# Kernel optimization log

Measured on AMD Instinct MI355X. Metric: run time of the kernel, lower is better.

The kernel has to match this reference:

```python
import jax, jax.numpy as jnp
import numpy as np


def _conv1d(x, kernel, bias):
    # Keras Conv1D, padding='valid', stride 1. x: (b, ts, c); kernel: (K, c, f)
    y = jax.lax.conv_general_dilated(x, kernel, (1,), 'VALID',
                                     dimension_numbers=('NWC', 'WIO', 'NWC'))
    return y + bias


def setup_inputs() -> dict:
    key = jax.random.key(0)
    k1, k2, k3 = jax.random.split(key, 3)
    KSIZE, C, F = 5, 32, 32
    x = jax.random.normal(k1, (16, 65536, C), jnp.float32)
    Wconv = jax.random.normal(k2, (KSIZE, C, F), jnp.float32) * 0.05
    bconv = jnp.zeros((F,), jnp.float32)
    Wdef = jax.random.normal(k3, (KSIZE, 1), jnp.float32) * 0.1
    return {"x": x, "Wconv": Wconv, "bconv": bconv, "Wdef": Wdef}


def reference(x, Wconv, bconv, Wdef):
    K = Wconv.shape[0]
    # regularGrid: R = [-floor(K/2), ..., K-1-floor(K/2)]
    R = jnp.arange(K, dtype=jnp.float32) - (K // 2)
    offset = _conv1d(x, Wconv, bconv)                 # (b, ts-K+1, f)
    # dpn = mean over all positions of (offset + R) -> mean(offset) + R, shape (K,)
    pn = jnp.mean(offset) + R
    # g(Q, Q+pn) = max(0, 1 - |Q - (Q+pn)|) = max(0, 1 - |pn|): constant per tap
    scale = jnp.maximum(0.0, 1.0 - jnp.abs(pn))       # (K,)
    # y_k = scale_k * flatten(x); sum_k W_k * y_k == x * sum_k(W_k * scale_k)
    s = jnp.sum(Wdef[:, 0] * scale)                   # scalar
    y = x * s                                         # (b, ts, c)
    return _conv1d(y, Wconv, bconv)                   # (b, ts-K+1, f)
```

## Files before the change

kernel.cpp:

```cpp
#include <hip/hip_runtime.h>
#include <hip/hip_fp16.h>

#define T    65536
#define TOUT 65532
#define NB   16
#define CH   32
#define NF   32
#define KS   5
#define BM   128
#define NCHB 1024

typedef _Float16 f16x8 __attribute__((ext_vector_type(8)));
typedef _Float16 f16x4 __attribute__((ext_vector_type(4)));
typedef float    f32x4 __attribute__((ext_vector_type(4)));
typedef float    f32x4v __attribute__((ext_vector_type(4)));


__device__ __forceinline__ f16x4 cvt4(float4 v) {
    f16x4 h;
    h[0] = (_Float16)v.x; h[1] = (_Float16)v.y;
    h[2] = (_Float16)v.z; h[3] = (_Float16)v.w;
    return h;
}
__device__ __forceinline__ f16x4 cvt4v(f32x4v v) {
    f16x4 h;
    h[0] = (_Float16)v[0]; h[1] = (_Float16)v[1];
    h[2] = (_Float16)v[2]; h[3] = (_Float16)v[3];
    return h;
}

template <bool WRITE_XH>
__global__ __launch_bounds__(256) void chsum6_kernel(const float* __restrict__ x,
                                                     _Float16* __restrict__ xh,
                                                     float* __restrict__ partials) {
    __shared__ float tot[CH];
    const int tid  = threadIdx.x;
    const int lane = tid & 63;
    if (tid < CH) tot[tid] = 0.f;
    __syncthreads();

    const f32x4v* x4  = (const f32x4v*)x;
    f16x4*        xh4 = (f16x4*)xh;
    const size_t base = (size_t)blockIdx.x * 8192;
    float s0 = 0.f, s1 = 0.f, s2 = 0.f, s3 = 0.f;
#pragma unroll 8
    for (int q = 0; q < 32; ++q) {
        size_t i = base + (size_t)q * 256 + tid;
        f32x4v v = __builtin_nontemporal_load(&x4[i]);
        s0 += v[0]; s1 += v[1]; s2 += v[2]; s3 += v[3];
        if (WRITE_XH) xh4[i] = cvt4v(v);
    }
#pragma unroll
    for (int m = 8; m <= 32; m <<= 1) {
        s0 += __shfl_xor(s0, m, 64);
        s1 += __shfl_xor(s1, m, 64);
        s2 += __shfl_xor(s2, m, 64);
        s3 += __shfl_xor(s3, m, 64);
    }
    if (lane < 8) {
        const int cc = lane * 4;
        atomicAdd(&tot[cc + 0], s0);
        atomicAdd(&tot[cc + 1], s1);
        atomicAdd(&tot[cc + 2], s2);
        atomicAdd(&tot[cc + 3], s3);
    }
    __syncthreads();
    if (tid < CH) partials[(size_t)blockIdx.x * CH + tid] = tot[tid];
}

__global__ __launch_bounds__(256) void scalar2_kernel(const float* __restrict__ x,
                                                      const float* __restrict__ Wconv,
                                                      const float* __restrict__ bconv,
                                                      const float* __restrict__ Wdef,
                                                      const float* __restrict__ partials,
                                                      float* __restrict__ ws) {
    __shared__ float ltot[CH];
    __shared__ float hb[4][CH], tb[4][CH];
    __shared__ float partial[256];
    const int tid = threadIdx.x;
    if (tid < CH) ltot[tid] = 0.f;
    __syncthreads();
    {
        const float4* p4 = (const float4*)partials;
        float s0 = 0.f, s1 = 0.f, s2 = 0.f, s3 = 0.f;
#pragma unroll 8
        for (int i = 0; i < 32; ++i) {
            float4 v = p4[i * 256 + tid];
            s0 += v.x; s1 += v.y; s2 += v.z; s3 += v.w;
        }
        int cc = (tid & 7) * 4;
        atomicAdd(&ltot[cc + 0], s0);
        atomicAdd(&ltot[cc + 1], s1);
        atomicAdd(&ltot[cc + 2], s2);
        atomicAdd(&ltot[cc + 3], s3);
    }
    {
        int j = tid >> 5, c = tid & 31;
        int row = (j < 4) ? j : (T - 8 + j);
        float e = 0.f;
        for (int bb = 0; bb < NB; ++bb)
            e += x[((size_t)bb * T + row) * CH + c];
        if (j < 4) hb[j][c] = e; else tb[j - 4][c] = e;
    }
    __syncthreads();

    float term = 0.f;
    if (tid < KS * CH) {
        int k = tid >> 5, c = tid & 31;
        float wf = 0.f;
        const float* wp = &Wconv[(size_t)tid * NF];
        for (int f = 0; f < NF; ++f) wf += wp[f];
        float S = ltot[c];
        for (int jj = 0; jj < k; ++jj) S -= hb[jj][c];
        for (int jj = k; jj < 4; ++jj) S -= tb[jj][c];
        term = wf * S;
    }
    partial[tid] = term;
    __syncthreads();
    for (int off = 128; off > 0; off >>= 1) {
        if (tid < off) partial[tid] += partial[tid + off];
        __syncthreads();
    }
    if (tid == 0) {
        float sum_b = 0.f;
        for (int f = 0; f < NF; ++f) sum_b += bconv[f];
        float mean_off = partial[0] / (float)((size_t)NB * TOUT * NF) + sum_b / (float)NF;
        float s = 0.f;
        for (int k = 0; k < KS; ++k) {
            float pn = mean_off + (float)(k - 2);
            s += Wdef[k] * fmaxf(0.f, 1.f - fabsf(pn));
        }
        ws[CH] = s;
    }
}

__global__ __launch_bounds__(256) void conv2_kernel(const _Float16* __restrict__ xh,
                                                    const float* __restrict__ Wconv,
                                                    const float* __restrict__ bconv,
                                                    const float* __restrict__ ws,
                                                    float* __restrict__ out) {
    __shared__ _Float16 A[(BM + 4) * 40];
    __shared__ _Float16 Wt[KS * CH * 40];

    const int tid = threadIdx.x;
    const int b   = blockIdx.y;
    const int t0  = blockIdx.x * BM;
    const int c0  = (tid & 7) * 4;

    {
        const f16x4* xh4 = (const f16x4*)xh;
        for (int r = (tid >> 3); r < BM + 4; r += 32) {
            int t = t0 + r;
            f16x4 h = {};
            if (t < T) h = xh4[((size_t)b * T + t) * 8 + (tid & 7)];
            *(f16x4*)&A[r * 40 + c0] = h;
        }
    }
    {
        const float4* w4 = (const float4*)Wconv;
#pragma unroll
        for (int j = 0; j < 5; ++j) {
            int i4 = tid + j * 256;
            float4 v = w4[i4];
            int fi = i4 * 4;
            int k = fi >> 10, c = (fi >> 5) & 31, f = fi & 31;
            _Float16* wrow = &Wt[(k * CH + f) * 40 + c];
            wrow[0 * 40] = (_Float16)v.x;
            wrow[1 * 40] = (_Float16)v.y;
            wrow[2 * 40] = (_Float16)v.z;
            wrow[3 * 40] = (_Float16)v.w;
        }
    }
    __syncthreads();

    const int lane = tid & 63;
    const int wave = tid >> 6;
    const int rowbase = wave * 32;
    const int lrow = lane & 15;
    const int kgrp = lane >> 4;

    f32x4 acc00 = {}, acc01 = {}, acc10 = {}, acc11 = {};
#pragma unroll
    for (int kk = 0; kk < KS; ++kk) {
        f16x8 a0 = *(const f16x8*)&A[(rowbase + lrow + kk) * 40 + kgrp * 8];
        f16x8 a1 = *(const f16x8*)&A[(rowbase + 16 + lrow + kk) * 40 + kgrp * 8];
        f16x8 b0 = *(const f16x8*)&Wt[(kk * CH + lrow) * 40 + kgrp * 8];
        f16x8 b1 = *(const f16x8*)&Wt[(kk * CH + 16 + lrow) * 40 + kgrp * 8];
        acc00 = __builtin_amdgcn_mfma_f32_16x16x32_f16(a0, b0, acc00, 0, 0, 0);
        acc01 = __builtin_amdgcn_mfma_f32_16x16x32_f16(a0, b1, acc01, 0, 0, 0);
        acc10 = __builtin_amdgcn_mfma_f32_16x16x32_f16(a1, b0, acc10, 0, 0, 0);
        acc11 = __builtin_amdgcn_mfma_f32_16x16x32_f16(a1, b1, acc11, 0, 0, 0);
    }

    float sv  = ws[CH];
    int col0  = lane & 15;
    float bc0 = bconv[col0], bc1 = bconv[col0 + 16];
    int rbase = rowbase + ((lane >> 4) << 2);
#pragma unroll
    for (int reg = 0; reg < 4; ++reg) {
        int t = t0 + rbase + reg;
        if (t < TOUT) {
            float* o = &out[((size_t)b * TOUT + t) * NF];
            o[col0]      = sv * acc00[reg] + bc0;
            o[col0 + 16] = sv * acc01[reg] + bc1;
        }
        int t1 = t + 16;
        if (t1 < TOUT) {
            float* o = &out[((size_t)b * TOUT + t1) * NF];
            o[col0]      = sv * acc10[reg] + bc0;
            o[col0 + 16] = sv * acc11[reg] + bc1;
        }
    }
}

__global__ __launch_bounds__(256) void conv_kernel(const float* __restrict__ x,
                                                   const float* __restrict__ Wconv,
                                                   const float* __restrict__ bconv,
                                                   const float* __restrict__ ws,
                                                   float* __restrict__ out) {
    __shared__ _Float16 A[(BM + 4) * 40];
    __shared__ _Float16 Wt[KS * CH * 40];
    int tid = threadIdx.x;
    int b   = blockIdx.y;
    int t0  = blockIdx.x * BM;
    {
        int c0 = (tid & 7) * 4;
        for (int r = (tid >> 3); r < BM + 4; r += 32) {
            int t = t0 + r;
            float4 v = make_float4(0.f, 0.f, 0.f, 0.f);
            if (t < T) v = *(const float4*)&x[((size_t)b * T + t) * CH + c0];
            *(f16x4*)&A[r * 40 + c0] = cvt4(v);
        }
    }
    if (tid < KS * CH) {
        int k = tid >> 5, c = tid & 31;
        const float* wp = &Wconv[(size_t)tid * NF];
        for (int f = 0; f < NF; ++f)
            Wt[(k * CH + f) * 40 + c] = (_Float16)wp[f];
    }
    __syncthreads();
    int lane = tid & 63;
    int wave = tid >> 6;
    int rowbase = wave * 32;
    int lrow = lane & 15;
    int kgrp = lane >> 4;
    f32x4 acc00 = {}, acc01 = {}, acc10 = {}, acc11 = {};
#pragma unroll
    for (int kk = 0; kk < KS; ++kk) {
        f16x8 a0 = *(const f16x8*)&A[(rowbase + lrow + kk) * 40 + kgrp * 8];
        f16x8 a1 = *(const f16x8*)&A[(rowbase + 16 + lrow + kk) * 40 + kgrp * 8];
        f16x8 b0 = *(const f16x8*)&Wt[(kk * CH + lrow) * 40 + kgrp * 8];
        f16x8 b1 = *(const f16x8*)&Wt[(kk * CH + 16 + lrow) * 40 + kgrp * 8];
        acc00 = __builtin_amdgcn_mfma_f32_16x16x32_f16(a0, b0, acc00, 0, 0, 0);
        acc01 = __builtin_amdgcn_mfma_f32_16x16x32_f16(a0, b1, acc01, 0, 0, 0);
        acc10 = __builtin_amdgcn_mfma_f32_16x16x32_f16(a1, b0, acc10, 0, 0, 0);
        acc11 = __builtin_amdgcn_mfma_f32_16x16x32_f16(a1, b1, acc11, 0, 0, 0);
    }
    float sv  = ws[CH];
    int col0  = lane & 15;
    float bc0 = bconv[col0], bc1 = bconv[col0 + 16];
    int rbase = rowbase + ((lane >> 4) << 2);
#pragma unroll
    for (int reg = 0; reg < 4; ++reg) {
        int t = t0 + rbase + reg;
        if (t < TOUT) {
            float* o = &out[((size_t)b * TOUT + t) * NF];
            o[col0]      = sv * acc00[reg] + bc0;
            o[col0 + 16] = sv * acc01[reg] + bc1;
        }
        int t1 = t + 16;
        if (t1 < TOUT) {
            float* o = &out[((size_t)b * TOUT + t1) * NF];
            o[col0]      = sv * acc10[reg] + bc0;
            o[col0 + 16] = sv * acc11[reg] + bc1;
        }
    }
}

extern "C" void kernel_launch(void* const* d_in, const int* in_sizes, int n_in,
                              void* d_out, int out_size, void* d_ws, size_t ws_size,
                              hipStream_t stream) {
    const float* x     = (const float*)d_in[0];
    const float* Wconv = (const float*)d_in[1];
    const float* bconv = (const float*)d_in[2];
    const float* Wdef  = (const float*)d_in[3];
    float* out      = (float*)d_out;
    float* ws       = (float*)d_ws;
    float* partials = ws + 64;
    _Float16* xh    = (_Float16*)((char*)d_ws + 524288);

    const size_t need = 524288 + (size_t)NB * T * CH * sizeof(_Float16);
    dim3 grid((TOUT + BM - 1) / BM, NB);

    if (ws_size >= need) {
        chsum6_kernel<true><<<dim3(NCHB), dim3(256), 0, stream>>>(x, xh, partials);
        scalar2_kernel<<<dim3(1), dim3(256), 0, stream>>>(x, Wconv, bconv, Wdef, partials, ws);
        conv2_kernel<<<grid, dim3(256), 0, stream>>>(xh, Wconv, bconv, ws, out);
    } else {
        chsum6_kernel<false><<<dim3(NCHB), dim3(256), 0, stream>>>(x, xh, partials);
        scalar2_kernel<<<dim3(1), dim3(256), 0, stream>>>(x, Wconv, bconv, Wdef, partials, ws);
        conv_kernel<<<grid, dim3(256), 0, stream>>>(x, Wconv, bconv, ws, out);
    }
}
```

Measured before the change: 80.62 us.

## Process two row tiles per conv block with register prefetch; double channel-sum blocks

Measured after the change: 78.53 us. -2.6%, faster.

```diff
diff --git a/kernel.cpp b/kernel.cpp
--- a/kernel.cpp
+++ b/kernel.cpp
@@ -8,7 +8,7 @@
 #define NF   32
 #define KS   5
 #define BM   128
-#define NCHB 1024
+#define NCHB 2048
 
 typedef _Float16 f16x8 __attribute__((ext_vector_type(8)));
 typedef _Float16 f16x4 __attribute__((ext_vector_type(4)));
@@ -41,10 +41,10 @@
 
     const f32x4v* x4  = (const f32x4v*)x;
     f16x4*        xh4 = (f16x4*)xh;
-    const size_t base = (size_t)blockIdx.x * 8192;
+    const size_t base = (size_t)blockIdx.x * 4096;
     float s0 = 0.f, s1 = 0.f, s2 = 0.f, s3 = 0.f;
 #pragma unroll 8
-    for (int q = 0; q < 32; ++q) {
+    for (int q = 0; q < 16; ++q) {
         size_t i = base + (size_t)q * 256 + tid;
         f32x4v v = __builtin_nontemporal_load(&x4[i]);
         s0 += v[0]; s1 += v[1]; s2 += v[2]; s3 += v[3];
@@ -84,7 +84,7 @@
         const float4* p4 = (const float4*)partials;
         float s0 = 0.f, s1 = 0.f, s2 = 0.f, s3 = 0.f;
 #pragma unroll 8
-        for (int i = 0; i < 32; ++i) {
+        for (int i = 0; i < 64; ++i) {
             float4 v = p4[i * 256 + tid];
             s0 += v.x; s1 += v.y; s2 += v.z; s3 += v.w;
         }
@@ -134,7 +134,7 @@
     }
 }
 
-__global__ __launch_bounds__(256) void conv2_kernel(const _Float16* __restrict__ xh,
+__global__ __launch_bounds__(256) void conv3_kernel(const _Float16* __restrict__ xh,
                                                     const float* __restrict__ Wconv,
                                                     const float* __restrict__ bconv,
                                                     const float* __restrict__ ws,
@@ -144,18 +144,36 @@
 
     const int tid = threadIdx.x;
     const int b   = blockIdx.y;
-    const int t0  = blockIdx.x * BM;
+    const int t0  = blockIdx.x * (2 * BM);
     const int c0  = (tid & 7) * 4;
-
-    {
-        const f16x4* xh4 = (const f16x4*)xh;
-        for (int r = (tid >> 3); r < BM + 4; r += 32) {
-            int t = t0 + r;
-            f16x4 h = {};
-            if (t < T) h = xh4[((size_t)b * T + t) * 8 + (tid & 7)];
-            *(f16x4*)&A[r * 40 + c0] = h;
-        }
-    }
+    const int g8  = tid & 7;
+    const int srow = tid >> 3;
+
+    const f16x4* xh4 = (const f16x4*)xh;
+    const size_t rowb = (size_t)b * T * 8;
+
+    f16x4 ra0, ra1, ra2, ra3, ra4;
+    auto LOADA = [&](int sub) {
+        int tbase = t0 + sub * BM + srow;
+        ra0 = xh4[rowb + (size_t)(tbase      ) * 8 + g8];
+        ra1 = xh4[rowb + (size_t)(tbase + 32 ) * 8 + g8];
+        ra2 = xh4[rowb + (size_t)(tbase + 64 ) * 8 + g8];
+        ra3 = xh4[rowb + (size_t)(tbase + 96 ) * 8 + g8];
+        if (tid < 32) {
+            int t = t0 + sub * BM + 128 + srow;
+            ra4 = (t < T) ? xh4[rowb + (size_t)t * 8 + g8] : (f16x4){};
+        }
+    };
+    auto WRITEA = [&]() {
+        *(f16x4*)&A[(srow      ) * 40 + c0] = ra0;
+        *(f16x4*)&A[(srow + 32 ) * 40 + c0] = ra1;
+        *(f16x4*)&A[(srow + 64 ) * 40 + c0] = ra2;
+        *(f16x4*)&A[(srow + 96 ) * 40 + c0] = ra3;
+        if (tid < 32)
+            *(f16x4*)&A[(128 + srow) * 40 + c0] = ra4;
+    };
+
+    LOADA(0);
     {
         const float4* w4 = (const float4*)Wconv;
 #pragma unroll
@@ -171,6 +189,7 @@
             wrow[3 * 40] = (_Float16)v.w;
         }
     }
+    WRITEA();
     __syncthreads();
 
     const int lane = tid & 63;
@@ -178,37 +197,48 @@
     const int rowbase = wave * 32;
     const int lrow = lane & 15;
     const int kgrp = lane >> 4;
-
-    f32x4 acc00 = {}, acc01 = {}, acc10 = {}, acc11 = {};
-#pragma unroll
-    for (int kk = 0; kk < KS; ++kk) {
-        f16x8 a0 = *(const f16x8*)&A[(rowbase + lrow + kk) * 40 + kgrp * 8];
-        f16x8 a1 = *(const f16x8*)&A[(rowbase + 16 + lrow + kk) * 40 + kgrp * 8];
-        f16x8 b0 = *(const f16x8*)&Wt[(kk * CH + lrow) * 40 + kgrp * 8];
-        f16x8 b1 = *(const f16x8*)&Wt[(kk * CH + 16 + lrow) * 40 + kgrp * 8];
-        acc00 = __builtin_amdgcn_mfma_f32_16x16x32_f16(a0, b0, acc00, 0, 0, 0);
-        acc01 = __builtin_amdgcn_mfma_f32_16x16x32_f16(a0, b1, acc01, 0, 0, 0);
-        acc10 = __builtin_amdgcn_mfma_f32_16x16x32_f16(a1, b0, acc10, 0, 0, 0);
-        acc11 = __builtin_amdgcn_mfma_f32_16x16x32_f16(a1, b1, acc11, 0, 0, 0);
-    }
-
-    float sv  = ws[CH];
-    int col0  = lane & 15;
-    float bc0 = bconv[col0], bc1 = bconv[col0 + 16];
-    int rbase = rowbase + ((lane >> 4) << 2);
-#pragma unroll
-    for (int reg = 0; reg < 4; ++reg) {
-        int t = t0 + rbase + reg;
-        if (t < TOUT) {
-            float* o = &out[((size_t)b * TOUT + t) * NF];
-            o[col0]      = sv * acc00[reg] + bc0;
-            o[col0 + 16] = sv * acc01[reg] + bc1;
-        }
-        int t1 = t + 16;
-        if (t1 < TOUT) {
-            float* o = &out[((size_t)b * TOUT + t1) * NF];
-            o[col0]      = sv * acc10[reg] + bc0;
-            o[col0 + 16] = sv * acc11[reg] + bc1;
+    const int col0 = lane & 15;
+    const float sv  = ws[CH];
+    const float bc0 = bconv[col0], bc1 = bconv[col0 + 16];
+
+#pragma unroll
+    for (int sub = 0; sub < 2; ++sub) {
+        if (sub == 0) LOADA(1);
+
+        f32x4 acc00 = {}, acc01 = {}, acc10 = {}, acc11 = {};
+#pragma unroll
+        for (int kk = 0; kk < KS; ++kk) {
+            f16x8 a0 = *(const f16x8*)&A[(rowbase + lrow + kk) * 40 + kgrp * 8];
+            f16x8 a1 = *(const f16x8*)&A[(rowbase + 16 + lrow + kk) * 40 + kgrp * 8];
+            f16x8 b0 = *(const f16x8*)&Wt[(kk * CH + lrow) * 40 + kgrp * 8];
+            f16x8 b1 = *(const f16x8*)&Wt[(kk * CH + 16 + lrow) * 40 + kgrp * 8];
+            acc00 = __builtin_amdgcn_mfma_f32_16x16x32_f16(a0, b0, acc00, 0, 0, 0);
+            acc01 = __builtin_amdgcn_mfma_f32_16x16x32_f16(a0, b1, acc01, 0, 0, 0);
+            acc10 = __builtin_amdgcn_mfma_f32_16x16x32_f16(a1, b0, acc10, 0, 0, 0);
+            acc11 = __builtin_amdgcn_mfma_f32_16x16x32_f16(a1, b1, acc11, 0, 0, 0);
+        }
+
+        int tsub  = t0 + sub * BM;
+        int rbase = rowbase + ((lane >> 4) << 2);
+#pragma unroll
+        for (int reg = 0; reg < 4; ++reg) {
+            int t = tsub + rbase + reg;
+            if (t < TOUT) {
+                float* o = &out[((size_t)b * TOUT + t) * NF];
+                o[col0]      = sv * acc00[reg] + bc0;
+                o[col0 + 16] = sv * acc01[reg] + bc1;
+            }
+            int t1 = t + 16;
+            if (t1 < TOUT) {
+                float* o = &out[((size_t)b * TOUT + t1) * NF];
+                o[col0]      = sv * acc10[reg] + bc0;
+                o[col0 + 16] = sv * acc11[reg] + bc1;
+            }
+        }
+        if (sub == 0) {
+            __syncthreads();
+            WRITEA();
+            __syncthreads();
         }
     }
 }
@@ -290,15 +320,16 @@
     _Float16* xh    = (_Float16*)((char*)d_ws + 524288);
 
     const size_t need = 524288 + (size_t)NB * T * CH * sizeof(_Float16);
-    dim3 grid((TOUT + BM - 1) / BM, NB);
 
     if (ws_size >= need) {
         chsum6_kernel<true><<<dim3(NCHB), dim3(256), 0, stream>>>(x, xh, partials);
         scalar2_kernel<<<dim3(1), dim3(256), 0, stream>>>(x, Wconv, bconv, Wdef, partials, ws);
-        conv2_kernel<<<grid, dim3(256), 0, stream>>>(xh, Wconv, bconv, ws, out);
+        dim3 grid((TOUT + 2 * BM - 1) / (2 * BM), NB);
+        conv3_kernel<<<grid, dim3(256), 0, stream>>>(xh, Wconv, bconv, ws, out);
     } else {
         chsum6_kernel<false><<<dim3(NCHB), dim3(256), 0, stream>>>(x, xh, partials);
         scalar2_kernel<<<dim3(1), dim3(256), 0, stream>>>(x, Wconv, bconv, Wdef, partials, ws);
+        dim3 grid((TOUT + BM - 1) / BM, NB);
         conv_kernel<<<grid, dim3(256), 0, stream>>>(x, Wconv, bconv, ws, out);
     }
 }
```
